# Optimization experiments

Measured on AMD Instinct MI355X. Metric: run time of the kernel, lower is better.

The kernel has to match this reference:

```python
import jax, jax.numpy as jnp
import numpy as np

V, D, H, T, L, M = 32000, 768, 12, 2048, 4, 64
HD = D // H
EPS = 1e-5


def _layer_norm(x, scale, bias):
    mu = x.mean(-1, keepdims=True)
    var = ((x - mu) ** 2).mean(-1, keepdims=True)
    return (x - mu) * jax.lax.rsqrt(var + EPS) * scale + bias


def setup_inputs() -> dict:
    key = jax.random.key(0)
    ks = jax.random.split(key, 12)
    f32 = jnp.float32
    inp = {
        "tokens": jax.random.randint(ks[0], (1, T), 0, V, dtype=jnp.int32),
        "emb": jax.random.normal(ks[1], (V, D), f32) * 0.05,
        "pos": jax.random.normal(ks[2], (T, D), f32) * 0.05,
        "mem": jax.random.normal(ks[3], (M, D), f32) * 0.05,
        "ln1_s": jnp.ones((L, D), f32),
        "ln1_b": jnp.zeros((L, D), f32),
        "wq": jax.random.normal(ks[4], (L, D, D), f32) * (D ** -0.5),
        "wk": jax.random.normal(ks[5], (L, D, D), f32) * (D ** -0.5),
        "wv": jax.random.normal(ks[6], (L, D, D), f32) * (D ** -0.5),
        "wo": jax.random.normal(ks[7], (L, D, D), f32) * (D ** -0.5),
        "ln2_s": jnp.ones((L, D), f32),
        "ln2_b": jnp.zeros((L, D), f32),
        "w1": jax.random.normal(ks[8], (L, 4 * D, D), f32) * (D ** -0.5),
        "b1": jnp.zeros((L, 4 * D), f32),
        "w2": jax.random.normal(ks[9], (L, D, 4 * D), f32) * ((4 * D) ** -0.5),
        "b2": jnp.zeros((L, D), f32),
        "lnm_s": jnp.ones((D,), f32),
        "lnm_b": jnp.zeros((D,), f32),
    }
    return inp


def reference(tokens, emb, pos, mem, ln1_s, ln1_b, wq, wk, wv, wo,
              ln2_s, ln2_b, w1, b1, w2, b2, lnm_s, lnm_b):
    B, Tt = tokens.shape
    x = emb[tokens] + pos[:Tt][None]                       # [B,T,D]
    x = jnp.concatenate([jnp.broadcast_to(mem, (B, M, D)), x], axis=1)  # [B,S,D]
    S = M + Tt
    causal = jnp.tril(jnp.ones((S, S), bool))              # [S,S]
    neg_inf = jnp.finfo(x.dtype).min
    scale = 1.0 / np.sqrt(HD)

    def block(h, p):
        l1s, l1b, Wq, Wk, Wv, Wo, l2s, l2b, W1, B1, W2, B2 = p
        n = _layer_norm(h, l1s, l1b)
        q = (n @ Wq.T).reshape(B, S, H, HD).transpose(0, 2, 1, 3)  # bhsd
        k = (n @ Wk.T).reshape(B, S, H, HD).transpose(0, 2, 1, 3)
        v = (n @ Wv.T).reshape(B, S, H, HD).transpose(0, 2, 1, 3)
        scores = jnp.einsum('bhqd,bhkd->bhqk', q, k) * scale
        scores = jnp.where(causal[None, None], scores, neg_inf)
        attn = jax.nn.softmax(scores, axis=-1)
        o = jnp.einsum('bhqk,bhkd->bhqd', attn, v)
        o = o.transpose(0, 2, 1, 3).reshape(B, S, D) @ Wo.T
        h = h + o
        n = _layer_norm(h, l2s, l2b)
        ff = jax.nn.gelu(n @ W1.T + B1, approximate=True) @ W2.T + B2
        return h + ff, None

    x, _ = jax.lax.scan(block, x, (ln1_s, ln1_b, wq, wk, wv, wo,
                                   ln2_s, ln2_b, w1, b1, w2, b2))
    x = _layer_norm(x, lnm_s, lnm_b)
    return x[:, -M:, :]
```

## Files before the change

kernel.cpp:

```cpp
#include <hip/hip_runtime.h>
#include <math.h>

#define S_TOT 2112
#define SPAD  2176
#define DMODEL 768
#define QKVLD 2304
#define NMEM 64
#define NHEAD 12
#define HDIM 64

typedef unsigned short ushort_t;
typedef __attribute__((ext_vector_type(8))) short short8;
typedef __attribute__((ext_vector_type(4))) float f32x4;

__device__ __forceinline__ ushort_t f2bf(float f) {
    unsigned int u = __builtin_bit_cast(unsigned int, f);
    u = (u + 0x7FFFu + ((u >> 16) & 1u)) >> 16;
    return (ushort_t)u;
}

#define WAIT_LGKM() __builtin_amdgcn_s_waitcnt(0xC07F)
#define BAR()       __builtin_amdgcn_s_barrier()

__global__ __launch_bounds__(256) void cvt6_kernel(
    const float* __restrict__ wq, const float* __restrict__ wk,
    const float* __restrict__ wv, const float* __restrict__ wo,
    const float* __restrict__ w1, const float* __restrict__ w2,
    ushort_t* __restrict__ wqkv, ushort_t* __restrict__ wob,
    ushort_t* __restrict__ w1b, ushort_t* __restrict__ w2b)
{
    const int DDv = (DMODEL * DMODEL) / 4;
    const int DFv = (DMODEL * 4 * DMODEL) / 4;
    int i = blockIdx.x * 256 + threadIdx.x;
    const float* src;
    ushort_t* dst;
    if (i < 3 * DDv) {
        if (i < DDv)          { src = wq + (size_t)i * 4; }
        else if (i < 2 * DDv) { src = wk + (size_t)(i - DDv) * 4; }
        else                  { src = wv + (size_t)(i - 2 * DDv) * 4; }
        dst = wqkv + (size_t)i * 4;
    } else if (i < 4 * DDv) {
        src = wo + (size_t)(i - 3 * DDv) * 4;
        dst = wob + (size_t)(i - 3 * DDv) * 4;
    } else if (i < 4 * DDv + DFv) {
        src = w1 + (size_t)(i - 4 * DDv) * 4;
        dst = w1b + (size_t)(i - 4 * DDv) * 4;
    } else {
        src = w2 + (size_t)(i - 4 * DDv - DFv) * 4;
        dst = w2b + (size_t)(i - 4 * DDv - DFv) * 4;
    }
    float4 v = *(const float4*)src;
    ushort4 o;
    o.x = f2bf(v.x); o.y = f2bf(v.y); o.z = f2bf(v.z); o.w = f2bf(v.w);
    *(ushort4*)dst = o;
}

__global__ __launch_bounds__(256) void embed_kernel(
    const int* __restrict__ tokens, const float* __restrict__ emb,
    const float* __restrict__ pos, const float* __restrict__ mem,
    float* __restrict__ x)
{
    int s = blockIdx.x;
    int tid = threadIdx.x;
    float* xr = x + (size_t)s * DMODEL;
    if (s >= S_TOT) {
        for (int d = tid; d < DMODEL; d += 256) xr[d] = 0.0f;
    } else if (s < NMEM) {
        const float* mr = mem + (size_t)s * DMODEL;
        for (int d = tid; d < DMODEL; d += 256) xr[d] = mr[d];
    } else {
        int t = s - NMEM;
        int tok = tokens[t];
        const float* er = emb + (size_t)tok * DMODEL;
        const float* pr = pos + (size_t)t * DMODEL;
        for (int d = tid; d < DMODEL; d += 256) xr[d] = er[d] + pr[d];
    }
}

template <typename OUT>
__global__ __launch_bounds__(256) void ln_kernel(
    const float* __restrict__ X, const float* __restrict__ g,
    const float* __restrict__ b, OUT* __restrict__ Y)
{
    __shared__ float red[256];
    int row = blockIdx.x, tid = threadIdx.x;
    const float* xr = X + (size_t)row * DMODEL;
    float v0 = xr[tid], v1 = xr[tid + 256], v2 = xr[tid + 512];
    red[tid] = v0 + v1 + v2;
    __syncthreads();
    for (int s = 128; s > 0; s >>= 1) {
        if (tid < s) red[tid] += red[tid + s];
        __syncthreads();
    }
    float mu = red[0] * (1.0f / 768.0f);
    __syncthreads();
    float d0 = v0 - mu, d1 = v1 - mu, d2 = v2 - mu;
    red[tid] = d0 * d0 + d1 * d1 + d2 * d2;
    __syncthreads();
    for (int s = 128; s > 0; s >>= 1) {
        if (tid < s) red[tid] += red[tid + s];
        __syncthreads();
    }
    float inv = rsqrtf(red[0] * (1.0f / 768.0f) + 1e-5f);
    OUT* yr = Y + (size_t)row * DMODEL;
    float o0 = d0 * inv * g[tid]       + b[tid];
    float o1 = d1 * inv * g[tid + 256] + b[tid + 256];
    float o2 = d2 * inv * g[tid + 512] + b[tid + 512];
    if constexpr (sizeof(OUT) == 2) {
        yr[tid] = f2bf(o0); yr[tid + 256] = f2bf(o1); yr[tid + 512] = f2bf(o2);
    } else {
        yr[tid] = o0; yr[tid + 256] = o1; yr[tid + 512] = o2;
    }
}

__global__ __launch_bounds__(256) void gemm_mfma(
    const ushort_t* __restrict__ A, const ushort_t* __restrict__ B,
    const float* __restrict__ bias, const float* __restrict__ resid,
    void* __restrict__ Cp, int K, int ldc, int ncol0, int act, int c_bf16)
{
    __shared__ ushort_t As[2][4096];
    __shared__ ushort_t Bs[2][4096];
    int tid = threadIdx.x;
    int l = tid & 63, w = tid >> 6;
    int wr = w >> 1, wc = w & 1;

    int gx = gridDim.x;
    int nwg = gx * gridDim.y;
    int orig = blockIdx.x + gx * blockIdx.y;
    int q = nwg >> 3, r = nwg & 7;
    int xcd = orig & 7, loc = orig >> 3;
    int swz = (xcd < r ? xcd * (q + 1) : r * (q + 1) + (xcd - r) * q) + loc;
    int m0 = (swz / gx) * 128, n0 = (swz % gx) * 128;

    int kz = blockIdx.z;
    int nsplit = gridDim.z;
    int Kc = K / nsplit;
    bool split = (nsplit > 1);

    int g = l & 3;
    int srow[2], swoff[2];
#pragma unroll
    for (int it = 0; it < 2; ++it) {
        int row = w * 32 + it * 16 + (l >> 2);
        srow[it] = row;
        swoff[it] = row * 64 + ((g ^ ((row >> 1) & 3)) << 4);
    }
    const ushort_t* Ap0 = A + (size_t)(m0 + srow[0]) * K + kz * Kc + g * 8;
    const ushort_t* Ap1 = A + (size_t)(m0 + srow[1]) * K + kz * Kc + g * 8;
    const ushort_t* Bp0 = B + (size_t)(n0 + srow[0]) * K + kz * Kc + g * 8;
    const ushort_t* Bp1 = B + (size_t)(n0 + srow[1]) * K + kz * Kc + g * 8;

    int kc = l >> 4, mr = l & 15;
    int aoff[4], boff[4];
#pragma unroll
    for (int i = 0; i < 4; ++i) {
        int rr = wr * 64 + i * 16 + mr;
        aoff[i] = rr * 64 + ((kc ^ ((rr >> 1) & 3)) << 4);
        rr = wc * 64 + i * 16 + mr;
        boff[i] = rr * 64 + ((kc ^ ((rr >> 1) & 3)) << 4);
    }

    f32x4 acc[4][4];
#pragma unroll
    for (int i = 0; i < 4; ++i)
#pragma unroll
        for (int j = 0; j < 4; ++j)
            acc[i][j] = (f32x4){0.f, 0.f, 0.f, 0.f};

    int nk = Kc >> 5;

    {
        short8 a0 = *(const short8*)Ap0;
        short8 a1 = *(const short8*)Ap1;
        short8 b0 = *(const short8*)Bp0;
        short8 b1 = *(const short8*)Bp1;
        *(short8*)((char*)As[0] + swoff[0]) = a0;
        *(short8*)((char*)As[0] + swoff[1]) = a1;
        *(short8*)((char*)Bs[0] + swoff[0]) = b0;
        *(short8*)((char*)Bs[0] + swoff[1]) = b1;
    }
    short8 oa0 = *(const short8*)(Ap0 + 32), oa1 = *(const short8*)(Ap1 + 32);
    short8 ob0 = *(const short8*)(Bp0 + 32), ob1 = *(const short8*)(Bp1 + 32);
    short8 ea0 = *(const short8*)(Ap0 + 64), ea1 = *(const short8*)(Ap1 + 64);
    short8 eb0 = *(const short8*)(Bp0 + 64), eb1 = *(const short8*)(Bp1 + 64);
    WAIT_LGKM(); BAR();

    for (int k = 0; k < nk; k += 2) {
        {
            const char* bA = (const char*)As[0];
            const char* bB = (const char*)Bs[0];
            short8 af[4], bfr[4];
#pragma unroll
            for (int i = 0; i < 4; ++i) {
                af[i]  = *(const short8*)(bA + aoff[i]);
                bfr[i] = *(const short8*)(bB + boff[i]);
            }
#pragma unroll
            for (int i = 0; i < 4; ++i)
#pragma unroll
                for (int j = 0; j < 4; ++j)
                    acc[i][j] = __builtin_amdgcn_mfma_f32_16x16x32_bf16(af[i], bfr[j], acc[i][j], 0, 0, 0);

            if (k + 1 < nk) {
                *(short8*)((char*)As[1] + swoff[0]) = oa0;
                *(short8*)((char*)As[1] + swoff[1]) = oa1;
                *(short8*)((char*)Bs[1] + swoff[0]) = ob0;
                *(short8*)((char*)Bs[1] + swoff[1]) = ob1;
                if (k + 3 < nk) {
                    int ko = (k + 3) << 5;
                    oa0 = *(const short8*)(Ap0 + ko);
                    oa1 = *(const short8*)(Ap1 + ko);
                    ob0 = *(const short8*)(Bp0 + ko);
                    ob1 = *(const short8*)(Bp1 + ko);
                }
            }
            WAIT_LGKM(); BAR();
        }
        if (k + 1 < nk) {
            const char* bA = (const char*)As[1];
            const char* bB = (const char*)Bs[1];
            short8 af[4], bfr[4];
#pragma unroll
            for (int i = 0; i < 4; ++i) {
                af[i]  = *(const short8*)(bA + aoff[i]);
                bfr[i] = *(const short8*)(bB + boff[i]);
            }
#pragma unroll
            for (int i = 0; i < 4; ++i)
#pragma unroll
                for (int j = 0; j < 4; ++j)
                    acc[i][j] = __builtin_amdgcn_mfma_f32_16x16x32_bf16(af[i], bfr[j], acc[i][j], 0, 0, 0);

            if (k + 2 < nk) {
                *(short8*)((char*)As[0] + swoff[0]) = ea0;
                *(short8*)((char*)As[0] + swoff[1]) = ea1;
                *(short8*)((char*)Bs[0] + swoff[0]) = eb0;
                *(short8*)((char*)Bs[0] + swoff[1]) = eb1;
                if (k + 4 < nk) {
                    int ko = (k + 4) << 5;
                    ea0 = *(const short8*)(Ap0 + ko);
                    ea1 = *(const short8*)(Ap1 + ko);
                    eb0 = *(const short8*)(Bp0 + ko);
                    eb1 = *(const short8*)(Bp1 + ko);
                }
            }
            WAIT_LGKM(); BAR();
        }
    }

    int lq = l >> 4;
#pragma unroll
    for (int i = 0; i < 4; ++i) {
#pragma unroll
        for (int rr = 0; rr < 4; ++rr) {
            int m = m0 + wr * 64 + i * 16 + lq * 4 + rr;
#pragma unroll
            for (int j = 0; j < 4; ++j) {
                int n = n0 + wc * 64 + j * 16 + mr;
                float v = acc[i][j][rr];
                if (bias && (!split || kz == 0)) v += bias[n];
                if (act) {
                    float u = v;
                    float t = 0.7978845608028654f * (u + 0.044715f * u * u * u);
                    v = u / (1.0f + __expf(-2.0f * t));
                }
                size_t idx = (size_t)m * ldc + ncol0 + n;
                if (split) {
                    atomicAdd((float*)Cp + idx, v);
                } else {
                    if (resid) v += resid[idx];
                    if (c_bf16) ((ushort_t*)Cp)[idx] = f2bf(v);
                    else        ((float*)Cp)[idx] = v;
                }
            }
        }
    }
}

__global__ __launch_bounds__(256) void attn_mfma(
    const ushort_t* __restrict__ qkv, ushort_t* __restrict__ att)
{
    __shared__ ushort_t Qs[64][72];
    __shared__ ushort_t Ks[2][64][72];
    __shared__ ushort_t Vt[2][64][72];
    __shared__ ushort_t Ps[64][72];

    int qt  = (int)gridDim.x - 1 - (int)blockIdx.x;
    int h   = blockIdx.y;
    int tid = threadIdx.x;
    int w = tid >> 6, lane = tid & 63;
    int quad = lane >> 4, l16 = lane & 15;
    int sr = lane;
    int dg = w;

    const size_t TSTRIDE = (size_t)64 * QKVLD;

    {
        const ushort_t* qp = qkv + (size_t)(qt * 64 + sr) * QKVLD + h * HDIM + dg * 16;
        *(short8*)&Qs[sr][dg * 16]     = *(const short8*)qp;
        *(short8*)&Qs[sr][dg * 16 + 8] = *(const short8*)(qp + 8);
    }

    const ushort_t* kp = qkv + (size_t)sr * QKVLD + DMODEL + h * HDIM + dg * 16;
    const ushort_t* vp = kp + DMODEL;
    short8 pk0 = *(const short8*)kp, pk1 = *(const short8*)(kp + 8);
    short8 pv0 = *(const short8*)vp, pv1 = *(const short8*)(vp + 8);
    kp += TSTRIDE; vp += TSTRIDE;

    *(short8*)&Ks[0][sr][dg * 16]     = pk0;
    *(short8*)&Ks[0][sr][dg * 16 + 8] = pk1;
#pragma unroll
    for (int j = 0; j < 8; ++j) Vt[0][dg * 16 + j][sr] = (ushort_t)pv0[j];
#pragma unroll
    for (int j = 0; j < 8; ++j) Vt[0][dg * 16 + 8 + j][sr] = (ushort_t)pv1[j];

    pk0 = *(const short8*)kp; pk1 = *(const short8*)(kp + 8);
    pv0 = *(const short8*)vp; pv1 = *(const short8*)(vp + 8);
    kp += TSTRIDE; vp += TSTRIDE;

    WAIT_LGKM(); BAR();

    short8 qf[2];
    qf[0] = *(const short8*)&Qs[w * 16 + l16][quad * 8];
    qf[1] = *(const short8*)&Qs[w * 16 + l16][32 + quad * 8];

    float mstate[4] = {-1e30f, -1e30f, -1e30f, -1e30f};
    float lstate[4] = {0.f, 0.f, 0.f, 0.f};
    f32x4 accO[4];
#pragma unroll
    for (int j = 0; j < 4; ++j) accO[j] = (f32x4){0.f, 0.f, 0.f, 0.f};

    for (int kt = 0; kt <= qt; ++kt) {
        int cb = kt & 1;

        f32x4 sacc[4];
#pragma unroll
        for (int nt = 0; nt < 4; ++nt) {
            sacc[nt] = (f32x4){0.f, 0.f, 0.f, 0.f};
            short8 kf0 = *(const short8*)&Ks[cb][nt * 16 + l16][quad * 8];
            short8 kf1 = *(const short8*)&Ks[cb][nt * 16 + l16][32 + quad * 8];
            sacc[nt] = __builtin_amdgcn_mfma_f32_16x16x32_bf16(qf[0], kf0, sacc[nt], 0, 0, 0);
            sacc[nt] = __builtin_amdgcn_mfma_f32_16x16x32_bf16(qf[1], kf1, sacc[nt], 0, 0, 0);
        }

        if (kt + 1 <= qt) {
            int nb = cb ^ 1;
            *(short8*)&Ks[nb][sr][dg * 16]     = pk0;
            *(short8*)&Ks[nb][sr][dg * 16 + 8] = pk1;
#pragma unroll
            for (int j = 0; j < 8; ++j) Vt[nb][dg * 16 + j][sr] = (ushort_t)pv0[j];
#pragma unroll
            for (int j = 0; j < 8; ++j) Vt[nb][dg * 16 + 8 + j][sr] = (ushort_t)pv1[j];
            pk0 = *(const short8*)kp; pk1 = *(const short8*)(kp + 8);
            pv0 = *(const short8*)vp; pv1 = *(const short8*)(vp + 8);
            kp += TSTRIDE; vp += TSTRIDE;
        }

        bool diag = (kt == qt);
        float s[4][4], rmax[4];
#pragma unroll
        for (int r = 0; r < 4; ++r) rmax[r] = -1e30f;
#pragma unroll
        for (int nt = 0; nt < 4; ++nt)
#pragma unroll
            for (int r = 0; r < 4; ++r) {
                float v = sacc[nt][r] * 0.125f;
                if (diag && (nt * 16 + l16) > (w * 16 + quad * 4 + r)) v = -1e30f;
                s[nt][r] = v;
                rmax[r] = fmaxf(rmax[r], v);
            }
#pragma unroll
        for (int r = 0; r < 4; ++r) {
            rmax[r] = fmaxf(rmax[r], __shfl_xor(rmax[r], 1));
            rmax[r] = fmaxf(rmax[r], __shfl_xor(rmax[r], 2));
            rmax[r] = fmaxf(rmax[r], __shfl_xor(rmax[r], 4));
            rmax[r] = fmaxf(rmax[r], __shfl_xor(rmax[r], 8));
        }
        float alpha[4];
#pragma unroll
        for (int r = 0; r < 4; ++r) {
            float mnew = fmaxf(mstate[r], rmax[r]);
            alpha[r] = __expf(mstate[r] - mnew);
            mstate[r] = mnew;
        }
        float rsum[4] = {0.f, 0.f, 0.f, 0.f};
#pragma unroll
        for (int nt = 0; nt < 4; ++nt)
#pragma unroll
            for (int r = 0; r < 4; ++r) {
                float p = __expf(s[nt][r] - mstate[r]);
                Ps[w * 16 + quad * 4 + r][nt * 16 + l16] = f2bf(p);
                rsum[r] += p;
            }
#pragma unroll
        for (int r = 0; r < 4; ++r) {
            rsum[r] += __shfl_xor(rsum[r], 1);
            rsum[r] += __shfl_xor(rsum[r], 2);
            rsum[r] += __shfl_xor(rsum[r], 4);
            rsum[r] += __shfl_xor(rsum[r], 8);
            lstate[r] = lstate[r] * alpha[r] + rsum[r];
        }
#pragma unroll
        for (int j = 0; j < 4; ++j)
#pragma unroll
            for (int r = 0; r < 4; ++r) accO[j][r] *= alpha[r];

        short8 pf0 = *(const short8*)&Ps[w * 16 + l16][quad * 8];
        short8 pf1 = *(const short8*)&Ps[w * 16 + l16][32 + quad * 8];
#pragma unroll
        for (int j = 0; j < 4; ++j) {
            short8 vf0 = *(const short8*)&Vt[cb][j * 16 + l16][quad * 8];
            short8 vf1 = *(const short8*)&Vt[cb][j * 16 + l16][32 + quad * 8];
            accO[j] = __builtin_amdgcn_mfma_f32_16x16x32_bf16(pf0, vf0, accO[j], 0, 0, 0);
            accO[j] = __builtin_amdgcn_mfma_f32_16x16x32_bf16(pf1, vf1, accO[j], 0, 0, 0);
        }

        WAIT_LGKM(); BAR();
    }

#pragma unroll
    for (int j = 0; j < 4; ++j)
#pragma unroll
        for (int r = 0; r < 4; ++r) {
            float o = accO[j][r] / lstate[r];
            att[(size_t)(qt * 64 + w * 16 + quad * 4 + r) * DMODEL + h * HDIM + j * 16 + l16] = f2bf(o);
        }
}

extern "C" void kernel_launch(void* const* d_in, const int* in_sizes, int n_in,
                              void* d_out, int out_size, void* d_ws, size_t ws_size,
                              hipStream_t stream) {
    const int*   tokens = (const int*)d_in[0];
    const float* emb    = (const float*)d_in[1];
    const float* pos    = (const float*)d_in[2];
    const float* mem    = (const float*)d_in[3];
    const float* ln1_s  = (const float*)d_in[4];
    const float* ln1_b  = (const float*)d_in[5];
    const float* wq     = (const float*)d_in[6];
    const float* wk     = (const float*)d_in[7];
    const float* wv     = (const float*)d_in[8];
    const float* wo     = (const float*)d_in[9];
    const float* ln2_s  = (const float*)d_in[10];
    const float* ln2_b  = (const float*)d_in[11];
    const float* w1     = (const float*)d_in[12];
    const float* b1     = (const float*)d_in[13];
    const float* w2     = (const float*)d_in[14];
    const float* b2     = (const float*)d_in[15];
    const float* lnm_s  = (const float*)d_in[16];
    const float* lnm_b  = (const float*)d_in[17];
    float* out = (float*)d_out;

    const int D = DMODEL, L = 4, FF = 4 * DMODEL, SP = SPAD;
    const int DD = D * D;
    const int DF = D * FF;

    float*    x    = (float*)d_ws;
    ushort_t* qkvb = (ushort_t*)(x + (size_t)SP * D);
    ushort_t* nbuf = qkvb + (size_t)SP * 3 * D;
    ushort_t* attb = nbuf + (size_t)SP * D;
    ushort_t* ffh  = attb + (size_t)SP * D;
    ushort_t* wqkv = ffh  + (size_t)SP * FF;
    ushort_t* wob  = wqkv + (size_t)3 * DD;
    ushort_t* w1b  = wob  + (size_t)DD;
    ushort_t* w2b  = w1b  + (size_t)DF;

    embed_kernel<<<SP, 256, 0, stream>>>(tokens, emb, pos, mem, x);

    dim3 gQKV(18, 17);
    dim3 gO(6, 17, 4);
    dim3 gF1(24, 17);
    dim3 gF2(6, 17, 4);
    dim3 gA(S_TOT / 64, NHEAD);
    const int cvtBlocks = (4 * DD + 2 * DF) / 1024;

    for (int l = 0; l < L; ++l) {
        cvt6_kernel<<<cvtBlocks, 256, 0, stream>>>(
            wq + (size_t)l * DD, wk + (size_t)l * DD, wv + (size_t)l * DD,
            wo + (size_t)l * DD, w1 + (size_t)l * DF, w2 + (size_t)l * DF,
            wqkv, wob, w1b, w2b);

        ln_kernel<ushort_t><<<SP, 256, 0, stream>>>(x, ln1_s + l * D, ln1_b + l * D, nbuf);
        gemm_mfma<<<gQKV, 256, 0, stream>>>(nbuf, wqkv, nullptr, nullptr,
                                            qkvb, D, 3 * D, 0, 0, 1);
        attn_mfma<<<gA, 256, 0, stream>>>(qkvb, attb);
        gemm_mfma<<<gO, 256, 0, stream>>>(attb, wob, nullptr, nullptr,
                                          x, D, D, 0, 0, 0);
        ln_kernel<ushort_t><<<SP, 256, 0, stream>>>(x, ln2_s + l * D, ln2_b + l * D, nbuf);
        gemm_mfma<<<gF1, 256, 0, stream>>>(nbuf, w1b, b1 + (size_t)l * FF, nullptr,
                                           ffh, D, FF, 0, 1, 1);
        gemm_mfma<<<gF2, 256, 0, stream>>>(ffh, w2b, b2 + (size_t)l * D, nullptr,
                                           x, FF, D, 0, 0, 0);
    }
    ln_kernel<float><<<NMEM, 256, 0, stream>>>(x + (size_t)(S_TOT - NMEM) * D,
                                               lnm_s, lnm_b, out);
}
```

Baseline: 1.086 ms.

## Split attention KV range into chunks and combine partial softmax results

Attention is split along the key dimension into up to four chunks of nine tiles each, launched as a third grid dimension. Each block writes its unnormalized bf16 partial output plus its running max and sum, and a new combine kernel merges them with log-sum-exp rescaling. This targets the load imbalance of causal attention, where the last query tiles iterate over 33 key tiles while only 396 blocks exist. The cost is an extra launch, traffic for the partial buffers (which reuse the ffh and nbuf scratch), and bf16 rounding of the unnormalized partials.

```diff
diff --git a/kernel.cpp b/kernel.cpp
--- a/kernel.cpp
+++ b/kernel.cpp
@@ -8,6 +8,9 @@
 #define NMEM 64
 #define NHEAD 12
 #define HDIM 64
+#define NQT 33
+#define CHUNK 9
+#define NZ 4
 
 typedef unsigned short ushort_t;
 typedef __attribute__((ext_vector_type(8))) short short8;
@@ -17,6 +20,10 @@
     unsigned int u = __builtin_bit_cast(unsigned int, f);
     u = (u + 0x7FFFu + ((u >> 16) & 1u)) >> 16;
     return (ushort_t)u;
+}
+__device__ __forceinline__ float bf2f(ushort_t u) {
+    unsigned int x = ((unsigned int)u) << 16;
+    return __builtin_bit_cast(float, x);
 }
 
 #define WAIT_LGKM() __builtin_amdgcn_s_waitcnt(0xC07F)
@@ -278,15 +285,21 @@
 }
 
 __global__ __launch_bounds__(256) void attn_mfma(
-    const ushort_t* __restrict__ qkv, ushort_t* __restrict__ att)
+    const ushort_t* __restrict__ qkv, ushort_t* __restrict__ Opart,
+    float* __restrict__ ml)
 {
     __shared__ ushort_t Qs[64][72];
     __shared__ ushort_t Ks[2][64][72];
     __shared__ ushort_t Vt[2][64][72];
     __shared__ ushort_t Ps[64][72];
 
-    int qt  = (int)gridDim.x - 1 - (int)blockIdx.x;
-    int h   = blockIdx.y;
+    int qt = blockIdx.x;
+    int h  = blockIdx.y;
+    int z  = blockIdx.z;
+    int kt0 = z * CHUNK;
+    if (kt0 > qt) return;
+    int kt1 = min(kt0 + CHUNK, qt + 1);
+
     int tid = threadIdx.x;
     int w = tid >> 6, lane = tid & 63;
     int quad = lane >> 4, l16 = lane & 15;
@@ -301,7 +314,7 @@
         *(short8*)&Qs[sr][dg * 16 + 8] = *(const short8*)(qp + 8);
     }
 
-    const ushort_t* kp = qkv + (size_t)sr * QKVLD + DMODEL + h * HDIM + dg * 16;
+    const ushort_t* kp = qkv + (size_t)(kt0 * 64 + sr) * QKVLD + DMODEL + h * HDIM + dg * 16;
     const ushort_t* vp = kp + DMODEL;
     short8 pk0 = *(const short8*)kp, pk1 = *(const short8*)(kp + 8);
     short8 pv0 = *(const short8*)vp, pv1 = *(const short8*)(vp + 8);
@@ -330,8 +343,8 @@
 #pragma unroll
     for (int j = 0; j < 4; ++j) accO[j] = (f32x4){0.f, 0.f, 0.f, 0.f};
 
-    for (int kt = 0; kt <= qt; ++kt) {
-        int cb = kt & 1;
+    for (int kt = kt0; kt < kt1; ++kt) {
+        int cb = (kt - kt0) & 1;
 
         f32x4 sacc[4];
 #pragma unroll
@@ -343,7 +356,7 @@
             sacc[nt] = __builtin_amdgcn_mfma_f32_16x16x32_bf16(qf[1], kf1, sacc[nt], 0, 0, 0);
         }
 
-        if (kt + 1 <= qt) {
+        if (kt + 1 < kt1) {
             int nb = cb ^ 1;
             *(short8*)&Ks[nb][sr][dg * 16]     = pk0;
             *(short8*)&Ks[nb][sr][dg * 16 + 8] = pk1;
@@ -418,13 +431,79 @@
         WAIT_LGKM(); BAR();
     }
 
+    size_t pidx = (size_t)(h * NQT + qt) * NZ + z;
 #pragma unroll
     for (int j = 0; j < 4; ++j)
 #pragma unroll
         for (int r = 0; r < 4; ++r) {
-            float o = accO[j][r] / lstate[r];
-            att[(size_t)(qt * 64 + w * 16 + quad * 4 + r) * DMODEL + h * HDIM + j * 16 + l16] = f2bf(o);
-        }
+            int row = w * 16 + quad * 4 + r;
+            Opart[pidx * 4096 + row * 64 + j * 16 + l16] = f2bf(accO[j][r]);
+        }
+    if (l16 == 0) {
+        float* mlr = ml + pidx * 128;
+#pragma unroll
+        for (int r = 0; r < 4; ++r) {
+            int row = w * 16 + quad * 4 + r;
+            mlr[row * 2]     = mstate[r];
+            mlr[row * 2 + 1] = lstate[r];
+        }
+    }
+}
+
+__global__ __launch_bounds__(256) void attn_combine(
+    const ushort_t* __restrict__ Opart, const float* __restrict__ ml,
+    ushort_t* __restrict__ att)
+{
+    int qt = blockIdx.x, h = blockIdx.y;
+    int nch = (qt + CHUNK) / CHUNK;
+    int t = threadIdx.x;
+    int row = t >> 2, c0 = (t & 3) << 4;
+    size_t pb = (size_t)(h * NQT + qt) * NZ;
+
+    float mv[NZ], lv[NZ];
+    float M = -1e30f;
+#pragma unroll
+    for (int z = 0; z < NZ; ++z) {
+        mv[z] = -1e30f; lv[z] = 0.f;
+        if (z < nch) {
+            const float* p = ml + (pb + z) * 128 + row * 2;
+            mv[z] = p[0]; lv[z] = p[1];
+            M = fmaxf(M, mv[z]);
+        }
+    }
+    float denom = 0.f;
+    float sc[NZ];
+#pragma unroll
+    for (int z = 0; z < NZ; ++z) {
+        sc[z] = 0.f;
+        if (z < nch) { sc[z] = __expf(mv[z] - M); denom += sc[z] * lv[z]; }
+    }
+    float inv = 1.0f / denom;
+
+    float o[16];
+#pragma unroll
+    for (int i = 0; i < 16; ++i) o[i] = 0.f;
+#pragma unroll
+    for (int z = 0; z < NZ; ++z) {
+        if (z < nch) {
+            const ushort_t* op = Opart + (pb + z) * 4096 + row * 64 + c0;
+            short8 a0 = *(const short8*)op;
+            short8 a1 = *(const short8*)(op + 8);
+#pragma unroll
+            for (int i = 0; i < 8; ++i) o[i]     += sc[z] * bf2f((ushort_t)a0[i]);
+#pragma unroll
+            for (int i = 0; i < 8; ++i) o[i + 8] += sc[z] * bf2f((ushort_t)a1[i]);
+        }
+    }
+    ushort_t* dst = att + (size_t)(qt * 64 + row) * DMODEL + h * HDIM + c0;
+    short8 r0, r1;
+#pragma unroll
+    for (int i = 0; i < 8; ++i) {
+        r0[i] = (short)f2bf(o[i] * inv);
+        r1[i] = (short)f2bf(o[i + 8] * inv);
+    }
+    *(short8*)dst = r0;
+    *(short8*)(dst + 8) = r1;
 }
 
 extern "C" void kernel_launch(void* const* d_in, const int* in_sizes, int n_in,
@@ -463,6 +542,8 @@
     ushort_t* wob  = wqkv + (size_t)3 * DD;
     ushort_t* w1b  = wob  + (size_t)DD;
     ushort_t* w2b  = w1b  + (size_t)DF;
+    ushort_t* Opart = ffh;
+    float*    mlbuf = (float*)nbuf;
 
     embed_kernel<<<SP, 256, 0, stream>>>(tokens, emb, pos, mem, x);
 
@@ -470,7 +551,8 @@
     dim3 gO(6, 17, 4);
     dim3 gF1(24, 17);
     dim3 gF2(6, 17, 4);
-    dim3 gA(S_TOT / 64, NHEAD);
+    dim3 gA(NQT, NHEAD, NZ);
+    dim3 gC(NQT, NHEAD);
     const int cvtBlocks = (4 * DD + 2 * DF) / 1024;
 
     for (int l = 0; l < L; ++l) {
@@ -482,7 +564,8 @@
         ln_kernel<ushort_t><<<SP, 256, 0, stream>>>(x, ln1_s + l * D, ln1_b + l * D, nbuf);
         gemm_mfma<<<gQKV, 256, 0, stream>>>(nbuf, wqkv, nullptr, nullptr,
                                             qkvb, D, 3 * D, 0, 0, 1);
-        attn_mfma<<<gA, 256, 0, stream>>>(qkvb, attb);
+        attn_mfma<<<gA, 256, 0, stream>>>(qkvb, Opart, mlbuf);
+        attn_combine<<<gC, 256, 0, stream>>>(Opart, mlbuf, attb);
         gemm_mfma<<<gO, 256, 0, stream>>>(attb, wob, nullptr, nullptr,
                                           x, D, D, 0, 0, 0);
         ln_kernel<ushort_t><<<SP, 256, 0, stream>>>(x, ln2_s + l * D, ln2_b + l * D, nbuf);
```

Result: faster. 1.015 ms (-6.6%).
